# Optimization experiments

Hardware: AMD Instinct MI355X
Metric: run time of the kernel (lower is better)

The kernel has to match this reference:

```python
import jax, jax.numpy as jnp
import numpy as np

B, S, D, H = 4, 2048, 1024, 16
DH = D // H  # 64


def setup_inputs() -> dict:
    key = jax.random.key(0)
    ks = jax.random.split(key, 11)
    s = 0.02
    return {
        "query": jax.random.normal(ks[0], (B, S, D), jnp.float32),
        "key": jax.random.normal(ks[1], (B, S, D), jnp.float32),
        "value": jax.random.normal(ks[2], (B, S, D), jnp.float32),
        "Wq": jax.random.normal(ks[3], (D, D), jnp.float32) * s,
        "bq": jnp.zeros((D,), jnp.float32),
        "Wk": jax.random.normal(ks[4], (D, D), jnp.float32) * s,
        "bk": jnp.zeros((D,), jnp.float32),
        "Wv": jax.random.normal(ks[5], (D, D), jnp.float32) * s,
        "bv": jnp.zeros((D,), jnp.float32),
        "Wo": jax.random.normal(ks[6], (D, D), jnp.float32) * s,
        "bo": jnp.zeros((D,), jnp.float32),
    }


def reference(query, key, value, Wq, bq, Wk, bk, Wv, bv, Wo, bo):
    b, s, _ = query.shape
    # linear projections (torch Linear: x @ W^T + b; here W stored as [in, out])
    q = query @ Wq + bq
    k = key @ Wk + bk
    v = value @ Wv + bv
    # split heads -> [B, H, S, DH]
    q = q.reshape(b, s, H, DH).transpose(0, 2, 1, 3)
    k = k.reshape(b, s, H, DH).transpose(0, 2, 1, 3)
    v = v.reshape(b, s, H, DH).transpose(0, 2, 1, 3)
    scale = jnp.sqrt(jnp.asarray(DH, jnp.float32))
    attn = jnp.einsum("bhqd,bhkd->bhqk", q, k) / scale  # [B,H,S,S]
    attn = jax.nn.softmax(attn, axis=-1)
    out = jnp.einsum("bhqk,bhkd->bhqd", attn, v)
    out = out.transpose(0, 2, 1, 3).reshape(b, s, D)
    return out @ Wo + bo
```

## Files before the change

### kernel.cpp

```cpp
#include <hip/hip_runtime.h>

typedef float f32x4 __attribute__((ext_vector_type(4)));
typedef __bf16 bf16x8 __attribute__((ext_vector_type(8)));
typedef unsigned short u16;
typedef unsigned int u32;
typedef u16 u16x4 __attribute__((ext_vector_type(4)));
typedef u16 u16x8 __attribute__((ext_vector_type(8)));
typedef u32 u32x2 __attribute__((ext_vector_type(2)));
typedef u32 u32x4 __attribute__((ext_vector_type(4)));

constexpr int Bn = 4, Sn = 2048, Dn = 1024, Hn = 16, DHn = 64;
constexpr int Mn = Bn * Sn;

static __device__ __forceinline__ u16 f2bf(float f) {
  return __builtin_bit_cast(u16, (__bf16)f);
}

static __device__ __forceinline__ u32 cvtpk(float lo, float hi) {
  u32 r;
  asm("v_cvt_pk_bf16_f32 %0, %1, %2" : "=v"(r) : "v"(lo), "v"(hi));
  return r;
}

static __device__ __forceinline__ void async16(const void* g, void* l) {
  __builtin_amdgcn_global_load_lds((const __attribute__((address_space(1))) u32*)g,
                                   (__attribute__((address_space(3))) u32*)l, 16, 0, 0);
}

static __device__ __forceinline__ void wait_bar2() {
  asm volatile("s_waitcnt vmcnt(2)" ::: "memory");
  __builtin_amdgcn_sched_barrier(0);
  __builtin_amdgcn_s_barrier();
  __builtin_amdgcn_sched_barrier(0);
}
static __device__ __forceinline__ void wait_bar4() {
  asm volatile("s_waitcnt vmcnt(4)" ::: "memory");
  __builtin_amdgcn_sched_barrier(0);
  __builtin_amdgcn_s_barrier();
  __builtin_amdgcn_sched_barrier(0);
}
static __device__ __forceinline__ void wait_bar8() {
  asm volatile("s_waitcnt vmcnt(8)" ::: "memory");
  __builtin_amdgcn_sched_barrier(0);
  __builtin_amdgcn_s_barrier();
  __builtin_amdgcn_sched_barrier(0);
}
static __device__ __forceinline__ void wait_bar0() {
  asm volatile("s_waitcnt vmcnt(0)" ::: "memory");
  __builtin_amdgcn_sched_barrier(0);
  __builtin_amdgcn_s_barrier();
  __builtin_amdgcn_sched_barrier(0);
}
static __device__ __forceinline__ void raw_bar() {
  __builtin_amdgcn_sched_barrier(0);
  __builtin_amdgcn_s_barrier();
  __builtin_amdgcn_sched_barrier(0);
}
static __device__ __forceinline__ void lgkm_bar() {
  asm volatile("s_waitcnt lgkmcnt(0)" ::: "memory");
  __builtin_amdgcn_sched_barrier(0);
  __builtin_amdgcn_s_barrier();
  __builtin_amdgcn_sched_barrier(0);
}

__global__ void __launch_bounds__(256) transpose4_kernel(const float* __restrict__ Wq,
                                                         const float* __restrict__ Wk,
                                                         const float* __restrict__ Wv,
                                                         const float* __restrict__ Wo,
                                                         u16* __restrict__ Wts) {
  __shared__ float tile[32][33];
  const int z = blockIdx.z;
  const float* W = (z == 0) ? Wq : (z == 1) ? Wk : (z == 2) ? Wv : Wo;
  u16* Wt = Wts + (size_t)z * Dn * Dn;
  const int n0 = blockIdx.x * 32, k0 = blockIdx.y * 32;
  const int tx = threadIdx.x & 31, ty = (threadIdx.x >> 5) * 4;
#pragma unroll
  for (int i = 0; i < 4; ++i)
    tile[ty + i][tx] = W[(size_t)(k0 + ty + i) * Dn + n0 + tx];
  __syncthreads();
#pragma unroll
  for (int i = 0; i < 4; ++i)
    Wt[(size_t)(n0 + ty + i) * Dn + k0 + tx] = f2bf(tile[tx][ty + i]);
}

__global__ void __launch_bounds__(256) gemm_qkv_kernel(const float* __restrict__ q_in,
                                                       const float* __restrict__ k_in,
                                                       const float* __restrict__ v_in,
                                                       const u16* __restrict__ Wts,
                                                       const float* __restrict__ bq,
                                                       const float* __restrict__ bk,
                                                       const float* __restrict__ bv,
                                                       u16* __restrict__ outbase) {
  __shared__ u16 As[2][128 * 64];
  __shared__ u16 Bs[2][128 * 64];

  const int bid = blockIdx.x;
  const int xcd = bid & 7;
  const int loc = bid >> 3;
  const int nb = loc & 7;
  const int panel = xcd * 24 + (loc >> 3);
  const int z = panel >> 6;
  const int m0 = (panel & 63) * 128, n0 = nb * 128;

  const float* A = (z == 0) ? q_in : (z == 1) ? k_in : v_in;
  const u16* Bt = Wts + (size_t)z * Dn * Dn;
  const float* bias = (z == 0) ? bq : (z == 1) ? bk : bv;
  u16* outp = outbase + (size_t)z * Mn * Dn;
  const float scale = (z == 0) ? 0.125f * 1.4426950408889634f : 1.0f;

  const int tid = threadIdx.x;
  const int wave = tid >> 6, lane = tid & 63;
  const int g = lane >> 4, c = lane & 15;
  const int wm = wave >> 1, wn = wave & 1;
  const int srow = lane >> 3, blk = lane & 7;

  f32x4 acc[4][4] = {};
  constexpr int NK = Dn / 64;

  f32x4 rA0lo[4], rA0hi[4], rA1lo[4], rA1hi[4];

  auto issueA = [&](int k0, f32x4 (&rlo)[4], f32x4 (&rhi)[4]) {
#pragma unroll
    for (int i = 0; i < 4; ++i) {
      const int row = (wave * 4 + i) * 8 + srow;
      const float* src = A + (size_t)(m0 + row) * Dn + k0 + blk * 8;
      rlo[i] = *(const f32x4*)src;
      rhi[i] = *(const f32x4*)(src + 4);
    }
  };
  auto writeA = [&](u16* dst, f32x4 (&rlo)[4], f32x4 (&rhi)[4]) {
#pragma unroll
    for (int i = 0; i < 4; ++i) {
      const int row = (wave * 4 + i) * 8 + srow;
      u32x4 w;
      w[0] = cvtpk(rlo[i][0], rlo[i][1]);
      w[1] = cvtpk(rlo[i][2], rlo[i][3]);
      w[2] = cvtpk(rhi[i][0], rhi[i][1]);
      w[3] = cvtpk(rhi[i][2], rhi[i][3]);
      *(u32x4*)(dst + row * 64 + ((blk ^ srow) * 8)) = w;
    }
  };
  auto issueB = [&](int k0, u16* dstB) {
#pragma unroll
    for (int i = 0; i < 4; ++i) {
      const int ch = wave * 4 + i, row = ch * 8 + srow, sb = blk ^ srow;
      async16(Bt + (size_t)(n0 + row) * Dn + k0 + sb * 8, dstB + ch * 512);
    }
  };
  auto mfma_tile = [&](const u16* Asb, const u16* Bsb) {
#pragma unroll
    for (int kk = 0; kk < 2; ++kk) {
      bf16x8 af[4], bfr[4];
#pragma unroll
      for (int mi = 0; mi < 4; ++mi)
        af[mi] = *(const bf16x8*)(Asb + (wm * 64 + mi * 16 + c) * 64 +
                                  (((kk * 4 + g) ^ (c & 7)) * 8));
#pragma unroll
      for (int ni = 0; ni < 4; ++ni)
        bfr[ni] = *(const bf16x8*)(Bsb + (wn * 64 + ni * 16 + c) * 64 +
                                   (((kk * 4 + g) ^ (c & 7)) * 8));
#pragma unroll
      for (int mi = 0; mi < 4; ++mi)
#pragma unroll
        for (int ni = 0; ni < 4; ++ni)
          acc[mi][ni] = __builtin_amdgcn_mfma_f32_16x16x32_bf16(af[mi], bfr[ni],
                                                                acc[mi][ni], 0, 0, 0);
    }
  };

  issueA(0, rA0lo, rA0hi);
  issueB(0, Bs[0]);
  asm volatile("s_waitcnt vmcnt(4)" ::: "memory");
  __builtin_amdgcn_sched_barrier(0);
  writeA(As[0], rA0lo, rA0hi);
  issueA(64, rA1lo, rA1hi);
  issueB(64, Bs[1]);
  asm volatile("s_waitcnt lgkmcnt(0)" ::: "memory");
  __builtin_amdgcn_sched_barrier(0);

  for (int kp = 0; kp < NK; kp += 2) {
    wait_bar4();
    if (kp + 2 < NK) issueA((kp + 2) * 64, rA0lo, rA0hi);
    writeA(As[1], rA1lo, rA1hi);
    mfma_tile(As[0], Bs[0]);
    lgkm_bar();
    if (kp + 2 < NK) issueB((kp + 2) * 64, Bs[0]);

    if (kp + 2 < NK) wait_bar4(); else wait_bar0();
    if (kp + 3 < NK) issueA((kp + 3) * 64, rA1lo, rA1hi);
    if (kp + 2 < NK) writeA(As[0], rA0lo, rA0hi);
    mfma_tile(As[1], Bs[1]);
    lgkm_bar();
    if (kp + 3 < NK) issueB((kp + 3) * 64, Bs[1]);
  }

  const bool vmode = (z == 2);
#pragma unroll
  for (int ni = 0; ni < 4; ++ni) {
    const int col = n0 + wn * 64 + ni * 16 + c;
    const float bv = bias[col];
    const int hh = col >> 6, dh = col & 63;
#pragma unroll
    for (int mi = 0; mi < 4; ++mi) {
      const int row = m0 + wm * 64 + mi * 16 + g * 4;
      const int bb = row >> 11, s = row & 2047;
      if (!vmode) {
        u16* o = outp + (((size_t)(bb * Hn + hh) * Sn + s) * DHn + dh);
#pragma unroll
        for (int r = 0; r < 4; ++r)
          o[(size_t)r * DHn] = f2bf((acc[mi][ni][r] + bv) * scale);
      } else {
        u16x4 pk;
#pragma unroll
        for (int r = 0; r < 4; ++r) pk[r] = f2bf(acc[mi][ni][r] + bv);
        *(u16x4*)(outp + ((size_t)(bb * Hn + hh) * DHn + dh) * Sn + s) = pk;
      }
    }
  }
}

__global__ void __launch_bounds__(256) gemm_o_kernel(const u16* __restrict__ A,
                                                     const u16* __restrict__ Bt,
                                                     const float* __restrict__ bias,
                                                     float* __restrict__ outp) {
  __shared__ u16 As[2][128 * 64];
  __shared__ u16 Bs[2][128 * 64];
  const int bid = blockIdx.x;
  const int xcd = bid & 7;
  const int loc = bid >> 3;
  const int nb = loc & 7;
  const int panel = xcd * 8 + (loc >> 3);
  const int m0 = panel * 128, n0 = nb * 128;

  const int tid = threadIdx.x;
  const int wave = tid >> 6, lane = tid & 63;
  const int g = lane >> 4, c = lane & 15;
  const int wm = wave >> 1, wn = wave & 1;
  const int srow = lane >> 3, blk = lane & 7;

  f32x4 acc[4][4] = {};
  constexpr int NK = Dn / 64;

#pragma unroll
  for (int p = 0; p < 2; ++p) {
    const int k0 = p * 64;
#pragma unroll
    for (int i = 0; i < 4; ++i) {
      const int ch = wave * 4 + i;
      const int row = ch * 8 + srow;
      const int sblk = blk ^ srow;
      async16(A + (size_t)(m0 + row) * Dn + k0 + sblk * 8, As[p] + ch * 512);
      async16(Bt + (size_t)(n0 + row) * Dn + k0 + sblk * 8, Bs[p] + ch * 512);
    }
  }

  for (int k = 0; k < NK; ++k) {
    const int cur = k & 1;
    if (k + 1 < NK) wait_bar8(); else wait_bar0();

#pragma unroll
    for (int kk = 0; kk < 2; ++kk) {
      bf16x8 af[4], bfr[4];
#pragma unroll
      for (int mi = 0; mi < 4; ++mi)
        af[mi] = *(const bf16x8*)(As[cur] + (wm * 64 + mi * 16 + c) * 64 +
                                  (((kk * 4 + g) ^ (c & 7)) * 8));
#pragma unroll
      for (int ni = 0; ni < 4; ++ni)
        bfr[ni] = *(const bf16x8*)(Bs[cur] + (wn * 64 + ni * 16 + c) * 64 +
                                   (((kk * 4 + g) ^ (c & 7)) * 8));
#pragma unroll
      for (int mi = 0; mi < 4; ++mi)
#pragma unroll
        for (int ni = 0; ni < 4; ++ni)
          acc[mi][ni] = __builtin_amdgcn_mfma_f32_16x16x32_bf16(af[mi], bfr[ni],
                                                                acc[mi][ni], 0, 0, 0);
    }

    raw_bar();
    if (k + 2 < NK) {
      const int k0 = (k + 2) * 64;
#pragma unroll
      for (int i = 0; i < 4; ++i) {
        const int ch = wave * 4 + i;
        const int row = ch * 8 + srow;
        const int sblk = blk ^ srow;
        async16(A + (size_t)(m0 + row) * Dn + k0 + sblk * 8, As[cur] + ch * 512);
        async16(Bt + (size_t)(n0 + row) * Dn + k0 + sblk * 8, Bs[cur] + ch * 512);
      }
    }
  }

#pragma unroll
  for (int ni = 0; ni < 4; ++ni) {
    const int col = n0 + wn * 64 + ni * 16 + c;
    const float bv = bias[col];
#pragma unroll
    for (int mi = 0; mi < 4; ++mi) {
      const int row = m0 + wm * 64 + mi * 16 + g * 4;
      float* o = outp + (size_t)row * Dn + col;
#pragma unroll
      for (int r = 0; r < 4; ++r) o[(size_t)r * Dn] = acc[mi][ni][r] + bv;
    }
  }
}

__global__ void __launch_bounds__(512, 4) attn_kernel(const u16* __restrict__ Q,
                                                      const u16* __restrict__ Kp,
                                                      const u16* __restrict__ VT,
                                                      u16* __restrict__ O) {
  __shared__ u16 Ks[3][64 * 64];
  __shared__ u16 Vs[3][64 * 64];
  const int tid = threadIdx.x;
  const int wave = tid >> 6, lane = tid & 63;
  const int g = lane >> 4, c = lane & 15;
  const int bh = blockIdx.x;
  const int q0 = blockIdx.y * 256 + wave * 32;
  const u16* Qb = Q + (size_t)bh * Sn * DHn;
  const u16* Kb = Kp + (size_t)bh * Sn * DHn;
  const u16* Vb = VT + (size_t)bh * DHn * Sn;

  bf16x8 qf[2][2];
#pragma unroll
  for (int fq = 0; fq < 2; ++fq)
#pragma unroll
    for (int kk = 0; kk < 2; ++kk)
      qf[fq][kk] = *(const bf16x8*)(Qb + (size_t)(q0 + fq * 16 + c) * DHn + kk * 32 + g * 8);

  f32x4 ot[4][2] = {};
  f32x4 lacc[2] = {};
  u16x8 one8u;
#pragma unroll
  for (int j = 0; j < 8; ++j) one8u[j] = 0x3F80;
  const bf16x8 one8 = __builtin_bit_cast(bf16x8, one8u);
  const f32x4 zf = {};

  const int srow = lane >> 3, blk = lane & 7;
  const int krow = wave * 8 + srow;
  const int sblk = blk ^ srow;
  constexpr int NT = Sn / 64;

  u16 *kA = Ks[0], *kB = Ks[1], *kC = Ks[2];
  u16 *vA = Vs[0], *vB = Vs[1], *vC = Vs[2];

#pragma unroll
  for (int tt = 0; tt < 2; ++tt) {
    const int kt = tt * 64;
    async16(Kb + (size_t)(kt + krow) * DHn + sblk * 8, Ks[tt] + wave * 512);
    async16(Vb + (size_t)krow * Sn + kt + sblk * 8, Vs[tt] + wave * 512);
  }

  for (int t = 0; t < NT; ++t) {
    if (t + 1 < NT) wait_bar2(); else wait_bar0();

    if (t + 2 < NT) {
      const int kt = (t + 2) * 64;
      async16(Kb + (size_t)(kt + krow) * DHn + sblk * 8, kC + wave * 512);
      async16(Vb + (size_t)krow * Sn + kt + sblk * 8, vC + wave * 512);
    }

    f32x4 st[4][2];
    {
      bf16x8 kf[4];
#pragma unroll
      for (int fk = 0; fk < 4; ++fk)
        kf[fk] = *(const bf16x8*)(kA + (fk * 16 + c) * 64 + ((g ^ (c & 7)) * 8));
      __builtin_amdgcn_s_setprio(1);
#pragma unroll
      for (int fk = 0; fk < 4; ++fk)
#pragma unroll
        for (int fq = 0; fq < 2; ++fq)
          st[fk][fq] = __builtin_amdgcn_mfma_f32_16x16x32_bf16(kf[fk], qf[fq][0],
                                                               zf, 0, 0, 0);
      __builtin_amdgcn_s_setprio(0);
#pragma unroll
      for (int fk = 0; fk < 4; ++fk)
        kf[fk] = *(const bf16x8*)(kA + (fk * 16 + c) * 64 + (((4 + g) ^ (c & 7)) * 8));
      __builtin_amdgcn_s_setprio(1);
#pragma unroll
      for (int fk = 0; fk < 4; ++fk)
#pragma unroll
        for (int fq = 0; fq < 2; ++fq)
          st[fk][fq] = __builtin_amdgcn_mfma_f32_16x16x32_bf16(kf[fk], qf[fq][1],
                                                               st[fk][fq], 0, 0, 0);
      __builtin_amdgcn_s_setprio(0);
    }

#pragma unroll
    for (int fq = 0; fq < 2; ++fq)
#pragma unroll
      for (int fk = 0; fk < 4; ++fk)
#pragma unroll
        for (int r = 0; r < 4; ++r)
          st[fk][fq][r] = __builtin_amdgcn_exp2f(st[fk][fq][r]);

    bf16x8 pf[2][2];
#pragma unroll
    for (int fq = 0; fq < 2; ++fq)
#pragma unroll
      for (int kk = 0; kk < 2; ++kk) {
        u32x4 pw;
#pragma unroll
        for (int w = 0; w < 2; ++w) {
          const u32 a = cvtpk(st[2 * kk][fq][2 * w], st[2 * kk][fq][2 * w + 1]);
          const u32 b = cvtpk(st[2 * kk + 1][fq][2 * w], st[2 * kk + 1][fq][2 * w + 1]);
          const u32x2 p1 = __builtin_amdgcn_permlane32_swap(a, b, false, false);
          const u32x2 p2 = __builtin_amdgcn_permlane16_swap(p1[0], p1[1], false, false);
          pw[w] = p2[0];
          pw[2 + w] = p2[1];
        }
        pf[kk][fq] = __builtin_bit_cast(bf16x8, pw);
      }

#pragma unroll
    for (int kk = 0; kk < 2; ++kk) {
      bf16x8 vf[4];
#pragma unroll
      for (int fa = 0; fa < 4; ++fa)
        vf[fa] = *(const bf16x8*)(vA + (fa * 16 + c) * 64 +
                                  (((kk * 4 + g) ^ (c & 7)) * 8));
      __builtin_amdgcn_s_setprio(1);
#pragma unroll
      for (int fa = 0; fa < 4; ++fa)
#pragma unroll
        for (int fq = 0; fq < 2; ++fq)
          ot[fa][fq] = __builtin_amdgcn_mfma_f32_16x16x32_bf16(vf[fa], pf[kk][fq],
                                                               ot[fa][fq], 0, 0, 0);
#pragma unroll
      for (int fq = 0; fq < 2; ++fq)
        lacc[fq] = __builtin_amdgcn_mfma_f32_16x16x32_bf16(one8, pf[kk][fq],
                                                           lacc[fq], 0, 0, 0);
      __builtin_amdgcn_s_setprio(0);
    }

    u16* tk = kA; kA = kB; kB = kC; kC = tk;
    u16* tv = vA; vA = vB; vB = vC; vC = tv;
  }

  const int bb = bh >> 4, hh = bh & 15;
#pragma unroll
  for (int fq = 0; fq < 2; ++fq) {
    const float inv = 1.f / lacc[fq][0];
    const int s = q0 + fq * 16 + c;
#pragma unroll
    for (int fa = 0; fa < 4; ++fa) {
      const int dh = fa * 16 + g * 4;
      u16x4 pk;
#pragma unroll
      for (int r = 0; r < 4; ++r) pk[r] = f2bf(ot[fa][fq][r] * inv);
      *(u16x4*)(O + ((size_t)bb * Sn + s) * Dn + hh * 64 + dh) = pk;
    }
  }
}

extern "C" void kernel_launch(void* const* d_in, const int* in_sizes, int n_in,
                              void* d_out, int out_size, void* d_ws, size_t ws_size,
                              hipStream_t stream) {
  (void)in_sizes; (void)n_in; (void)out_size; (void)ws_size;
  const float* q_in = (const float*)d_in[0];
  const float* k_in = (const float*)d_in[1];
  const float* v_in = (const float*)d_in[2];
  const float* Wq = (const float*)d_in[3];
  const float* bq = (const float*)d_in[4];
  const float* Wk = (const float*)d_in[5];
  const float* bk = (const float*)d_in[6];
  const float* Wv = (const float*)d_in[7];
  const float* bv = (const float*)d_in[8];
  const float* Wo = (const float*)d_in[9];
  const float* bo = (const float*)d_in[10];

  char* ws = (char*)d_ws;
  const size_t szX = (size_t)Mn * Dn * 2;
  const size_t szW = (size_t)Dn * Dn * 2;
  u16* Wts = (u16*)ws;
  u16* Qb = (u16*)(ws + 4 * szW + 0 * szX);
  u16* Kb = (u16*)(ws + 4 * szW + 1 * szX);
  u16* VTb = (u16*)(ws + 4 * szW + 2 * szX);
  u16* Ob = (u16*)(ws + 4 * szW + 3 * szX);

  transpose4_kernel<<<dim3(32, 32, 4), 256, 0, stream>>>(Wq, Wk, Wv, Wo, Wts);

  gemm_qkv_kernel<<<1536, 256, 0, stream>>>(q_in, k_in, v_in, Wts, bq, bk, bv, Qb);

  attn_kernel<<<dim3(Bn * Hn, Sn / 256), 512, 0, stream>>>(Qb, Kb, VTb, Ob);

  gemm_o_kernel<<<512, 256, 0, stream>>>(Ob, Wts + (size_t)3 * Dn * Dn, bo,
                                         (float*)d_out);
}
```

Measured before the change: 173.4 us.

## Triple-buffer B tiles in QKV GEMM to remove a barrier per k-step

```diff
diff --git a/kernel.cpp b/kernel.cpp
--- a/kernel.cpp
+++ b/kernel.cpp
@@ -33,12 +33,6 @@
   __builtin_amdgcn_s_barrier();
   __builtin_amdgcn_sched_barrier(0);
 }
-static __device__ __forceinline__ void wait_bar4() {
-  asm volatile("s_waitcnt vmcnt(4)" ::: "memory");
-  __builtin_amdgcn_sched_barrier(0);
-  __builtin_amdgcn_s_barrier();
-  __builtin_amdgcn_sched_barrier(0);
-}
 static __device__ __forceinline__ void wait_bar8() {
   asm volatile("s_waitcnt vmcnt(8)" ::: "memory");
   __builtin_amdgcn_sched_barrier(0);
@@ -56,8 +50,14 @@
   __builtin_amdgcn_s_barrier();
   __builtin_amdgcn_sched_barrier(0);
 }
-static __device__ __forceinline__ void lgkm_bar() {
-  asm volatile("s_waitcnt lgkmcnt(0)" ::: "memory");
+static __device__ __forceinline__ void qkv_wait4() {
+  asm volatile("s_waitcnt vmcnt(4) lgkmcnt(0)" ::: "memory");
+  __builtin_amdgcn_sched_barrier(0);
+  __builtin_amdgcn_s_barrier();
+  __builtin_amdgcn_sched_barrier(0);
+}
+static __device__ __forceinline__ void qkv_wait0() {
+  asm volatile("s_waitcnt vmcnt(0) lgkmcnt(0)" ::: "memory");
   __builtin_amdgcn_sched_barrier(0);
   __builtin_amdgcn_s_barrier();
   __builtin_amdgcn_sched_barrier(0);
@@ -92,7 +92,7 @@
                                                        const float* __restrict__ bv,
                                                        u16* __restrict__ outbase) {
   __shared__ u16 As[2][128 * 64];
-  __shared__ u16 Bs[2][128 * 64];
+  __shared__ u16 Bs[3][128 * 64];
 
   const int bid = blockIdx.x;
   const int xcd = bid & 7;
@@ -159,39 +159,50 @@
       for (int ni = 0; ni < 4; ++ni)
         bfr[ni] = *(const bf16x8*)(Bsb + (wn * 64 + ni * 16 + c) * 64 +
                                    (((kk * 4 + g) ^ (c & 7)) * 8));
+      __builtin_amdgcn_s_setprio(1);
 #pragma unroll
       for (int mi = 0; mi < 4; ++mi)
 #pragma unroll
         for (int ni = 0; ni < 4; ++ni)
           acc[mi][ni] = __builtin_amdgcn_mfma_f32_16x16x32_bf16(af[mi], bfr[ni],
                                                                 acc[mi][ni], 0, 0, 0);
+      __builtin_amdgcn_s_setprio(0);
     }
   };
 
+  u16 *bA = Bs[0], *bB = Bs[1], *bC = Bs[2];
+
   issueA(0, rA0lo, rA0hi);
-  issueB(0, Bs[0]);
+  issueB(0, bA);
   asm volatile("s_waitcnt vmcnt(4)" ::: "memory");
   __builtin_amdgcn_sched_barrier(0);
   writeA(As[0], rA0lo, rA0hi);
   issueA(64, rA1lo, rA1hi);
-  issueB(64, Bs[1]);
-  asm volatile("s_waitcnt lgkmcnt(0)" ::: "memory");
-  __builtin_amdgcn_sched_barrier(0);
+  issueB(64, bB);
 
   for (int kp = 0; kp < NK; kp += 2) {
-    wait_bar4();
-    if (kp + 2 < NK) issueA((kp + 2) * 64, rA0lo, rA0hi);
-    writeA(As[1], rA1lo, rA1hi);
-    mfma_tile(As[0], Bs[0]);
-    lgkm_bar();
-    if (kp + 2 < NK) issueB((kp + 2) * 64, Bs[0]);
-
-    if (kp + 2 < NK) wait_bar4(); else wait_bar0();
-    if (kp + 3 < NK) issueA((kp + 3) * 64, rA1lo, rA1hi);
-    if (kp + 2 < NK) writeA(As[0], rA0lo, rA0hi);
-    mfma_tile(As[1], Bs[1]);
-    lgkm_bar();
-    if (kp + 3 < NK) issueB((kp + 3) * 64, Bs[1]);
+    {
+      const int t = kp;
+      if (t + 1 < NK) qkv_wait4(); else qkv_wait0();
+      if (t + 2 < NK) {
+        issueA((t + 2) * 64, rA0lo, rA0hi);
+        issueB((t + 2) * 64, bC);
+      }
+      if (t + 1 < NK) writeA(As[1], rA1lo, rA1hi);
+      mfma_tile(As[0], bA);
+      u16* tb = bA; bA = bB; bB = bC; bC = tb;
+    }
+    {
+      const int t = kp + 1;
+      if (t + 1 < NK) qkv_wait4(); else qkv_wait0();
+      if (t + 2 < NK) {
+        issueA((t + 2) * 64, rA1lo, rA1hi);
+        issueB((t + 2) * 64, bC);
+      }
+      if (t + 1 < NK) writeA(As[0], rA0lo, rA0hi);
+      mfma_tile(As[1], bA);
+      u16* tb = bA; bA = bB; bB = bC; bC = tb;
+    }
   }
 
   const bool vmode = (z == 2);
```

Result: no change. 173.1 us (-0.2%).
